# Optimization experiments

Measured on AMD Instinct MI355X. Metric: run time of the kernel, lower is better.

## Reference

```python
import jax, jax.numpy as jnp
import numpy as np


def _pairwise_sq(x, y):
    # squared euclidean distances [B,N,M] via gram trick (avoids [B,N,M,D] temp)
    x2 = jnp.sum(x * x, -1)[:, :, None]
    y2 = jnp.sum(y * y, -1)[:, None, :]
    return x2 + y2 - 2.0 * jnp.einsum('bnd,bmd->bnm', x, y)


def _dtw_dp(C):
    # Subsequence DTW accumulated-cost matrix. C: [N,M].
    # D[0,:] = C[0,:] (free start anywhere in y);
    # D[i,j] = C[i,j] + min(D[i-1,j], D[i-1,j-1], D[i,j-1]).
    # Within-row recurrence D[i,j] = min(a[j], D[i,j-1] + C[i,j]) with
    # a[j] = min(D[i-1,j], D[i-1,j-1]) + C[i,j] is a min-plus prefix scan:
    # D[i,j] = S[j] + cummin(a - S)[j], S = cumsum(C[i]).
    inf = jnp.asarray(jnp.inf, C.dtype)
    def row(Dprev, Crow):
        shifted = jnp.concatenate([jnp.full((1,), inf, C.dtype), Dprev[:-1]])
        a = jnp.minimum(Dprev, shifted) + Crow
        S = jnp.cumsum(Crow)
        D = S + jax.lax.cummin(a - S)
        return D, D
    _, Dr = jax.lax.scan(row, C[0], C[1:])
    return jnp.concatenate([C[0][None], Dr], 0)


def _backtrack(D):
    # Backtrack optimal subseq-DTW path from (N-1, argmin D[-1]) to row 0.
    # Returns, per x index i, the largest y index aligned to i on the path
    # (== last occurrence kept by dict(dtw_path) in the torch code).
    N, M = D.shape
    inf = jnp.asarray(jnp.inf, D.dtype)
    j0 = jnp.argmin(D[-1]).astype(jnp.int32)
    i0 = jnp.asarray(N - 1, jnp.int32)
    yl = jnp.zeros((N,), jnp.int32).at[i0].set(j0)
    def step(carry, _):
        i, j, yl = carry
        dd = jnp.where(j > 0, D[i - 1, j - 1], inf)
        du = D[i - 1, j]
        dl = jnp.where(j > 0, D[i, j - 1], inf)
        best = jnp.minimum(jnp.minimum(dd, du), dl)
        take_d = dd == best
        take_u = (~take_d) & (du == best)
        ni = jnp.where(take_d | take_u, i - 1, i)
        nj = jnp.where(take_d, j - 1, jnp.where(take_u, j, j - 1))
        active = i > 0
        ni = jnp.where(active, ni, i)
        nj = jnp.where(active, nj, j)
        yl = jnp.where(active, yl.at[ni].max(nj), yl)
        return (ni, nj, yl), None
    (_, _, yl), _ = jax.lax.scan(step, (i0, j0, yl), None, length=N + M)
    return yl


def setup_inputs() -> dict:
    key = jax.random.key(0)
    k0, k1, k2, k3 = jax.random.split(key, 4)
    B, N, M, D = 16, 1024, 4096, 64
    return {
        'x': jax.random.normal(k0, (B, N, D), jnp.float32),
        'y': jax.random.normal(k1, (B, M, D), jnp.float32),
        'x_t': jax.random.uniform(k2, (B, N), dtype=jnp.float32),
        'y_t': jax.random.uniform(k3, (B, M), dtype=jnp.float32),
    }


def reference(x, y, x_t, y_t):
    C = _pairwise_sq(x, y)                      # [B,N,M]
    D = jax.vmap(_dtw_dp)(C)                    # [B,N,M]
    # total path cost == DP optimum (sum of C along the optimal path)
    dtw_cost = jnp.min(D[:, -1, :], axis=-1)    # [B]
    y_last = jax.vmap(_backtrack)(jax.lax.stop_gradient(D))  # [B,N] int32
    w_ts = x_t                                  # path covers all x indices 0..N-1 in order
    w_vs = jnp.take_along_axis(y_t, y_last, axis=1)
    return dtw_cost, w_ts, w_vs
```

## Files before the change

### kernel.cpp

```cpp
#include <hip/hip_runtime.h>

#define B_ 16
#define N_ 1024
#define M_ 4096
#define D_ 64
#define SROWS_ (N_ + 63)
#define SROWSP_ (SROWS_ + 17)
#define SPAIR_ 544
#define TSB_ ((size_t)SPAIR_ * 128)
#define BTQ_ 96
#define BTROWS_ 128
#define GEMM_BLKS_ 2048

__device__ __forceinline__ float finf() { return __builtin_inff(); }

__device__ __forceinline__ float wave_shr1(float x) {
  return __int_as_float(__builtin_amdgcn_update_dpp(
      0, __float_as_int(x), 0x138, 0xF, 0xF, false));
}
__device__ __forceinline__ float rdlane(float v, int l) {
  return __int_as_float(__builtin_amdgcn_readlane(__float_as_int(v), l));
}

__global__ void prep_kernel(const float* __restrict__ x,
                            const float* __restrict__ x_t,
                            float* __restrict__ x2,
                            float* __restrict__ w_ts_out,
                            int* __restrict__ ctrl) {
  int id = blockIdx.x * blockDim.x + threadIdx.x;
  if (ctrl && blockIdx.x == 0 && threadIdx.x < 128)
    ctrl[threadIdx.x] = (threadIdx.x < 64) ? 0 : -1;
  const float4* xr = (const float4*)(x + (size_t)id * D_);
  float s = 0.f;
#pragma unroll
  for (int e = 0; e < D_ / 4; ++e) {
    float4 v = xr[e];
    s += v.x * v.x + v.y * v.y + v.z * v.z + v.w * v.w;
  }
  x2[id] = s;
  w_ts_out[id] = x_t[id];
}

__device__ __forceinline__ void gemm_body(
    const float* __restrict__ x, const float* __restrict__ y,
    const float* __restrict__ x2, float* __restrict__ CsT, int jcol0,
    int b, int ibeg, int t, char* smem) {
  float4* ylds = (float4*)smem;
  float4* xlds = (float4*)(smem + 65536);
  float* y2lds = (float*)(smem + 73728);

  const int cg = t & 63;
  const int rg = t >> 6;
  {
    const int j = jcol0 + t;
    const float4* yrow = (const float4*)(y + ((size_t)b * M_ + j) * D_);
    float4 yr[16];
#pragma unroll
    for (int e = 0; e < 16; ++e) yr[e] = yrow[e];
    float y2 = 0.f;
#pragma unroll
    for (int e = 0; e < 16; ++e)
      y2 += yr[e].x * yr[e].x + yr[e].y * yr[e].y + yr[e].z * yr[e].z +
            yr[e].w * yr[e].w;
    y2lds[t] = y2;
#pragma unroll
    for (int e = 0; e < 16; ++e) ylds[e * 256 + t] = yr[e];
  }
  if (t < 128) {
    const int row = t >> 2;
    const int part = t & 3;
    const float4* xr = (const float4*)(x + ((size_t)b * N_ + ibeg + row) * D_);
#pragma unroll
    for (int k = 0; k < 4; ++k) {
      const int e = part * 4 + k;
      xlds[e * 32 + row] = xr[e];
    }
  }
  __syncthreads();

  const int r0 = rg * 8;
  float acc[8][4];
#pragma unroll
  for (int r = 0; r < 8; ++r)
#pragma unroll
    for (int c = 0; c < 4; ++c) acc[r][c] = 0.f;

#pragma unroll
  for (int kb = 0; kb < 4; ++kb) {
    float4 yf[4][4];
#pragma unroll
    for (int c = 0; c < 4; ++c)
#pragma unroll
      for (int ee = 0; ee < 4; ++ee)
        yf[c][ee] = ylds[(kb * 4 + ee) * 256 + cg + 64 * c];
#pragma unroll
    for (int r = 0; r < 8; ++r) {
      float4 xv[4];
#pragma unroll
      for (int ee = 0; ee < 4; ++ee)
        xv[ee] = xlds[(kb * 4 + ee) * 32 + r0 + r];
#pragma unroll
      for (int ee = 0; ee < 4; ++ee) {
#pragma unroll
        for (int c = 0; c < 4; ++c) {
          acc[r][c] += xv[ee].x * yf[c][ee].x + xv[ee].y * yf[c][ee].y +
                       xv[ee].z * yf[c][ee].z + xv[ee].w * yf[c][ee].w;
        }
      }
    }
  }

#pragma unroll
  for (int r = 0; r < 8; ++r) {
    const int i = ibeg + r0 + r;
    const float xx = x2[b * N_ + i];
#pragma unroll
    for (int c = 0; c < 4; ++c) {
      const int ct = cg + 64 * c;
      const int l = ct >> 2;
      CsT[(size_t)(i + l) * 256 + ct] = xx + y2lds[ct] - 2.f * acc[r][c];
    }
  }
}

__global__ __launch_bounds__(256) void gemm_kernel(
    const float* __restrict__ x, const float* __restrict__ y,
    const float* __restrict__ x2, float* __restrict__ Cs, int chunkBase,
    int nt, int tileOff) {
  __shared__ __align__(16) char smem[74752];
  const int tile = blockIdx.x;
  const int b = blockIdx.z;
  float* CsT =
      Cs + ((size_t)b * nt + tileOff + tile) * SROWSP_ * 256;
  gemm_body(x, y, x2, CsT, chunkBase + tile * 256, b, blockIdx.y * 32,
            threadIdx.x, smem);
}

__global__ __launch_bounds__(256) void dtw_pipe(
    const float* __restrict__ x, const float* __restrict__ y,
    const float* __restrict__ x2, float* __restrict__ Cs,
    unsigned char* __restrict__ dec, float* __restrict__ carryPipe,
    int* __restrict__ gemmCnt, int* __restrict__ carryProg,
    float* __restrict__ partV, int* __restrict__ partJ) {
  __shared__ __align__(16) char smem[90112];
  const int bid = blockIdx.x;
  const int t = threadIdx.x;

  if (bid >= 64) {
    const int gb = bid - 64;
    const int chunk = 1 + (gb >> 11);
    const int g2 = gb & 2047;
    const int b = g2 >> 7;
    const int tile = g2 & 3;
    const int ibeg = ((g2 >> 2) & 31) * 32;
    float* CsT =
        Cs + ((size_t)b * 16 + chunk * 4 + tile) * SROWSP_ * 256;
    gemm_body(x, y, x2, CsT, chunk * 1024 + tile * 256, b, ibeg, t, smem);
    __syncthreads();
    if (t == 0) {
      __threadfence();
      atomicAdd(&gemmCnt[b * 4 + chunk], 1);
    }
    return;
  }

  const int b = bid >> 2;
  const int C = bid & 3;
  const int lane = t & 63;
  const int W = t >> 6;

  float(*ring)[1024] = reinterpret_cast<float(*)[1024]>(smem);
  int* prog = reinterpret_cast<int*>(smem + 12288);
  float* redV = reinterpret_cast<float*>(smem + 12352);
  int* redJ = reinterpret_cast<int*>(smem + 12384);
  volatile int* vProg = prog;

  if (t < 3) prog[t] = -1;

  if (C > 0) {
    if (t == 0) {
      while (__hip_atomic_load(&gemmCnt[b * 4 + C], __ATOMIC_ACQUIRE,
                               __HIP_MEMORY_SCOPE_AGENT) < 128)
        __builtin_amdgcn_s_sleep(8);
      __threadfence();
    }
    __syncthreads();
  } else {
    __syncthreads();
  }

  const float INF = finf();
  const float* loadP = Cs + ((size_t)b * 16 + C * 4 + W) * SROWSP_ * 256;
  const int tileG = C * 4 + W;
  unsigned short* decP =
      (unsigned short*)(dec + (size_t)(b * 16 + tileG) * TSB_) + lane;
  const float* carryIn = carryPipe + ((size_t)b * 3 + (C > 0 ? C - 1 : 0)) * N_;
  float* carryOut = carryPipe + ((size_t)b * 3 + (C < 3 ? C : 0)) * N_;
  int* progIn = &carryProg[b * 4 + (C > 0 ? C - 1 : 0)];
  int* progOut = &carryProg[b * 4 + C];
  const int jbase = tileG * 256 + lane * 4;

  float4 cc0 = ((const float4*)(loadP + 0 * 256))[lane];
  float4 cc1 = ((const float4*)(loadP + 1 * 256))[lane];
  float4 cc2 = ((const float4*)(loadP + 2 * 256))[lane];
  float4 cc3 = ((const float4*)(loadP + 3 * 256))[lane];
  float4 cc4 = ((const float4*)(loadP + 4 * 256))[lane];
  float4 cc5 = ((const float4*)(loadP + 5 * 256))[lane];
  float4 cc6 = ((const float4*)(loadP + 6 * 256))[lane];
  float4 cc7 = ((const float4*)(loadP + 7 * 256))[lane];
  loadP += 8 * 256;

  float edgeVec = INF, lvPrev = INF;
  float up0 = 0.f, up1 = 0.f, up2 = 0.f, up3 = 0.f;
  float dpp1 = INF, dpp2 = INF;
  float fin0 = INF, fin1 = INF, fin2 = INF, fin3 = INF;
  float ebuf[8];

#define BLOCKHEADP()                                                          \
  {                                                                           \
    if (W > 0) {                                                              \
      if (sb < N_) {                                                          \
        const int tgt = sb + 7;                                               \
        while (vProg[W - 1] < tgt) {}                                         \
        asm volatile("" ::: "memory");                                        \
        lvPrev = rdlane(edgeVec, 7);                                          \
        edgeVec = ring[W - 1][(sb + lane) & 1023];                            \
      }                                                                       \
    } else if (C > 0) {                                                       \
      if (((sb & 63) == 0) && sb < N_) {                                      \
        const int tgt = sb + 63;                                              \
        if (lane == 0) {                                                      \
          while (__hip_atomic_load(progIn, __ATOMIC_ACQUIRE,                  \
                                   __HIP_MEMORY_SCOPE_AGENT) < tgt)           \
            __builtin_amdgcn_s_sleep(4);                                      \
        }                                                                     \
        edgeVec = carryIn[(sb + lane) & 1023];                                \
      }                                                                       \
    }                                                                         \
  }

#define DPSTEP(KK, CCV, ROW0, FIN)                                            \
  {                                                                           \
    const float lv = rdlane(edgeVec, eb + (KK));                              \
    const float left = (lane == 0) ? lv : dpp1;                               \
    const float diag = (lane == 0) ? lvPrev : dpp2;                           \
    lvPrev = lv;                                                              \
    float bv0 = fminf(diag, fminf(up0, left));                                \
    unsigned int pk = (diag <= bv0) ? 0u : ((up0 <= bv0) ? 1u : 2u);          \
    if (ROW0) bv0 = (sb + (KK) == lane) ? 0.f : bv0;                          \
    const float D0 = CCV.x + bv0;                                             \
    float bv1 = fminf(up0, fminf(up1, D0));                                   \
    pk |= (up0 <= bv1) ? 0u : ((up1 <= bv1) ? 4u : 8u);                       \
    if (ROW0) bv1 = (sb + (KK) == lane) ? 0.f : bv1;                          \
    const float D1 = CCV.y + bv1;                                             \
    float bv2 = fminf(up1, fminf(up2, D1));                                   \
    pk |= (up1 <= bv2) ? 0u : ((up2 <= bv2) ? 16u : 32u);                     \
    if (ROW0) bv2 = (sb + (KK) == lane) ? 0.f : bv2;                          \
    const float D2 = CCV.z + bv2;                                             \
    float bv3 = fminf(up2, fminf(up3, D2));                                   \
    pk |= (up2 <= bv3) ? 0u : ((up3 <= bv3) ? 64u : 128u);                    \
    if (ROW0) bv3 = (sb + (KK) == lane) ? 0.f : bv3;                          \
    const float D3 = CCV.w + bv3;                                             \
    ebuf[(KK)] = D3;                                                          \
    if ((KK) & 1) {                                                           \
      pk16 |= pk << 8;                                                        \
      decP[((KK) >> 1) * 64] = (unsigned short)pk16;                          \
    } else {                                                                  \
      pk16 = pk;                                                              \
    }                                                                         \
    if (FIN) {                                                                \
      const bool lr = (sb + (KK) == 1023 + lane);                             \
      fin0 = lr ? D0 : fin0; fin1 = lr ? D1 : fin1;                           \
      fin2 = lr ? D2 : fin2; fin3 = lr ? D3 : fin3;                           \
    }                                                                         \
    const float sh = wave_shr1(D3);                                           \
    dpp2 = dpp1; dpp1 = sh;                                                   \
    up0 = D0; up1 = D1; up2 = D2; up3 = D3;                                   \
    CCV = ((const float4*)(loadP + (KK) * 256))[lane];                        \
  }

#define BLOCKENDP()                                                           \
  {                                                                           \
    const int r0 = sb - 63;                                                   \
    if (W < 3) {                                                              \
      if (lane == 63 && r0 > -8 && r0 < N_) {                                 \
        _Pragma("unroll") for (int k = 0; k < 8; ++k) {                       \
          const int r = r0 + k;                                               \
          if ((unsigned)r < (unsigned)N_) ring[W][r] = ebuf[k];               \
        }                                                                     \
        __builtin_amdgcn_s_waitcnt(0xC07F);                                   \
        vProg[W] = r0 + 7;                                                    \
      }                                                                       \
    } else if (C < 3) {                                                       \
      if (lane == 63) {                                                       \
        if (r0 > -8 && r0 < N_) {                                             \
          _Pragma("unroll") for (int k = 0; k < 8; ++k) {                     \
            const int r = r0 + k;                                             \
            if ((unsigned)r < (unsigned)N_) carryOut[r] = ebuf[k];            \
          }                                                                   \
        }                                                                     \
        if ((sb & 63) == 56)                                                  \
          __hip_atomic_store(progOut, sb - 56, __ATOMIC_RELEASE,              \
                             __HIP_MEMORY_SCOPE_AGENT);                       \
      }                                                                       \
    }                                                                         \
    loadP += 8 * 256;                                                         \
    decP += 256;                                                              \
  }

#define STEP8(R0, FN)                                                         \
  DPSTEP(0, cc0, R0, FN) DPSTEP(1, cc1, R0, FN) DPSTEP(2, cc2, R0, FN)        \
  DPSTEP(3, cc3, R0, FN) DPSTEP(4, cc4, R0, FN) DPSTEP(5, cc5, R0, FN)        \
  DPSTEP(6, cc6, R0, FN) DPSTEP(7, cc7, R0, FN)

  int sb = 0;
  for (; sb < 64; sb += 8) {
    BLOCKHEADP();
    const int eb = (W == 0) ? (sb & 56) : 0;
    unsigned int pk16;
    STEP8(1, 0)
    BLOCKENDP();
  }
  for (; sb < 1016; sb += 8) {
    BLOCKHEADP();
    const int eb = (W == 0) ? (sb & 56) : 0;
    unsigned int pk16;
    STEP8(0, 0)
    BLOCKENDP();
  }
  for (; sb < 1088; sb += 8) {
    BLOCKHEADP();
    const int eb = (W == 0) ? (sb & 56) : 0;
    unsigned int pk16;
    STEP8(0, 1)
    BLOCKENDP();
  }
#undef DPSTEP
#undef STEP8
#undef BLOCKHEADP
#undef BLOCKENDP

  float mv = fin0; int mj = jbase;
  if (fin1 < mv) { mv = fin1; mj = jbase + 1; }
  if (fin2 < mv) { mv = fin2; mj = jbase + 2; }
  if (fin3 < mv) { mv = fin3; mj = jbase + 3; }
#pragma unroll
  for (int off = 32; off > 0; off >>= 1) {
    const float ov = __shfl_down(mv, off);
    const int oj = __shfl_down(mj, off);
    if (ov < mv || (ov == mv && oj < mj)) { mv = ov; mj = oj; }
  }
  if (lane == 0) { redV[W] = mv; redJ[W] = mj; }
  __syncthreads();
  if (t == 0) {
    float bm = redV[0]; int bj = redJ[0];
#pragma unroll
    for (int w = 1; w < 4; ++w)
      if (redV[w] < bm) { bm = redV[w]; bj = redJ[w]; }
    partV[b * 4 + C] = bm;
    partJ[b * 4 + C] = bj;
  }
}

__global__ __launch_bounds__(256) void dtw_fused(
    const float* __restrict__ x, const float* __restrict__ y,
    const float* __restrict__ x2, const float* __restrict__ CsRead,
    float* __restrict__ CsWrite, int nextBase,
    unsigned char* __restrict__ dec, const float* __restrict__ carryIn,
    float* __restrict__ carryOut, float* __restrict__ partV,
    int* __restrict__ partJ, int chunk, int hasCarry) {
  __shared__ __align__(16) char smem[90112];
  const int bid = blockIdx.x;
  const int t = threadIdx.x;

  if (bid >= B_) {
    const int gb = bid - B_;
    const int b = gb >> 7;
    const int tile = gb & 3;
    const int ibeg = ((gb >> 2) & 31) * 32;
    float* CsT = CsWrite + ((size_t)b * 4 + tile) * SROWSP_ * 256;
    gemm_body(x, y, x2, CsT, nextBase + tile * 256, b, ibeg, t, smem);
    return;
  }

  float(*ring)[1024] = reinterpret_cast<float(*)[1024]>(smem);
  float* cring = reinterpret_cast<float*>(smem + 12288);
  int* prog = reinterpret_cast<int*>(smem + 16384);
  float* redV = reinterpret_cast<float*>(smem + 16400);
  int* redJ = reinterpret_cast<int*>(smem + 16416);
  volatile int* vProg = prog;

  const int b = bid;
  const int lane = t & 63;
  const int W = t >> 6;

  if (t < 3) prog[t] = -1;
  const float* cIn = carryIn + b * N_;
  if (hasCarry) ((float4*)cring)[t] = ((const float4*)cIn)[t];
  __syncthreads();

  const float INF = finf();
  const float* loadP = CsRead + (size_t)(b * 4 + W) * SROWSP_ * 256;
  const int tileG = chunk * 4 + W;
  unsigned short* decP =
      (unsigned short*)(dec + (size_t)(b * 16 + tileG) * TSB_) + lane;
  float* carryB = carryOut + b * N_;
  const int jbase = tileG * 256 + lane * 4;

  float4 cc0 = ((const float4*)(loadP + 0 * 256))[lane];
  float4 cc1 = ((const float4*)(loadP + 1 * 256))[lane];
  float4 cc2 = ((const float4*)(loadP + 2 * 256))[lane];
  float4 cc3 = ((const float4*)(loadP + 3 * 256))[lane];
  float4 cc4 = ((const float4*)(loadP + 4 * 256))[lane];
  float4 cc5 = ((const float4*)(loadP + 5 * 256))[lane];
  float4 cc6 = ((const float4*)(loadP + 6 * 256))[lane];
  float4 cc7 = ((const float4*)(loadP + 7 * 256))[lane];
  loadP += 8 * 256;

  float edgeVec = INF, lvPrev = INF;
  float up0 = 0.f, up1 = 0.f, up2 = 0.f, up3 = 0.f;
  float dpp1 = INF, dpp2 = INF;
  float fin0 = INF, fin1 = INF, fin2 = INF, fin3 = INF;
  float ebuf[8];

#define BLOCKHEAD()                                                           \
  {                                                                           \
    if (W > 0) {                                                              \
      if (sb < N_) {                                                          \
        const int tgt = sb + 7;                                               \
        while (vProg[W - 1] < tgt) {}                                         \
        asm volatile("" ::: "memory");                                        \
        lvPrev = rdlane(edgeVec, 7);                                          \
        edgeVec = ring[W - 1][(sb + lane) & 1023];                            \
      }                                                                       \
    } else if (hasCarry) {                                                    \
      lvPrev = rdlane(edgeVec, 7);                                            \
      if (sb < N_) edgeVec = cring[(sb + lane) & 1023];                       \
    }                                                                         \
  }

#define DPSTEP(KK, CCV, ROW0, FIN)                                            \
  {                                                                           \
    const float lv = rdlane(edgeVec, (KK));                                   \
    const float left = (lane == 0) ? lv : dpp1;                               \
    const float diag = (lane == 0) ? lvPrev : dpp2;                           \
    lvPrev = lv;                                                              \
    float bv0 = fminf(diag, fminf(up0, left));                                \
    unsigned int pk = (diag <= bv0) ? 0u : ((up0 <= bv0) ? 1u : 2u);          \
    if (ROW0) bv0 = (sb + (KK) == lane) ? 0.f : bv0;                          \
    const float D0 = CCV.x + bv0;                                             \
    float bv1 = fminf(up0, fminf(up1, D0));                                   \
    pk |= (up0 <= bv1) ? 0u : ((up1 <= bv1) ? 4u : 8u);                       \
    if (ROW0) bv1 = (sb + (KK) == lane) ? 0.f : bv1;                          \
    const float D1 = CCV.y + bv1;                                             \
    float bv2 = fminf(up1, fminf(up2, D1));                                   \
    pk |= (up1 <= bv2) ? 0u : ((up2 <= bv2) ? 16u : 32u);                     \
    if (ROW0) bv2 = (sb + (KK) == lane) ? 0.f : bv2;                          \
    const float D2 = CCV.z + bv2;                                             \
    float bv3 = fminf(up2, fminf(up3, D2));                                   \
    pk |= (up2 <= bv3) ? 0u : ((up3 <= bv3) ? 64u : 128u);                    \
    if (ROW0) bv3 = (sb + (KK) == lane) ? 0.f : bv3;                          \
    const float D3 = CCV.w + bv3;                                             \
    ebuf[(KK)] = D3;                                                          \
    if ((KK) & 1) {                                                           \
      pk16 |= pk << 8;                                                        \
      decP[((KK) >> 1) * 64] = (unsigned short)pk16;                          \
    } else {                                                                  \
      pk16 = pk;                                                              \
    }                                                                         \
    if (FIN) {                                                                \
      const bool lr = (sb + (KK) == 1023 + lane);                             \
      fin0 = lr ? D0 : fin0; fin1 = lr ? D1 : fin1;                           \
      fin2 = lr ? D2 : fin2; fin3 = lr ? D3 : fin3;                           \
    }                                                                         \
    const float sh = wave_shr1(D3);                                           \
    dpp2 = dpp1; dpp1 = sh;                                                   \
    up0 = D0; up1 = D1; up2 = D2; up3 = D3;                                   \
    CCV = ((const float4*)(loadP + (KK) * 256))[lane];                        \
  }

#define BLOCKEND()                                                            \
  {                                                                           \
    const int r0 = sb - 63;                                                   \
    if (W < 3) {                                                              \
      if (lane == 63 && r0 > -8 && r0 < N_) {                                 \
        _Pragma("unroll") for (int k = 0; k < 8; ++k) {                       \
          const int r = r0 + k;                                               \
          if ((unsigned)r < (unsigned)N_) ring[W][r] = ebuf[k];               \
        }                                                                     \
        __builtin_amdgcn_s_waitcnt(0xC07F);                                   \
        vProg[W] = r0 + 7;                                                    \
      }                                                                       \
    } else if (chunk < 3) {                                                   \
      if (lane == 63 && r0 > -8 && r0 < N_) {                                 \
        _Pragma("unroll") for (int k = 0; k < 8; ++k) {                       \
          const int r = r0 + k;                                               \
          if ((unsigned)r < (unsigned)N_) carryB[r] = ebuf[k];                \
        }                                                                     \
      }                                                                       \
    }                                                                         \
    loadP += 8 * 256;                                                         \
    decP += 256;                                                              \
  }

#define STEP8(R0, FN)                                                         \
  DPSTEP(0, cc0, R0, FN) DPSTEP(1, cc1, R0, FN) DPSTEP(2, cc2, R0, FN)        \
  DPSTEP(3, cc3, R0, FN) DPSTEP(4, cc4, R0, FN) DPSTEP(5, cc5, R0, FN)        \
  DPSTEP(6, cc6, R0, FN) DPSTEP(7, cc7, R0, FN)

  int sb = 0;
  for (; sb < 64; sb += 8) {
    BLOCKHEAD();
    unsigned int pk16;
    STEP8(1, 0)
    BLOCKEND();
  }
  for (; sb < 1016; sb += 8) {
    BLOCKHEAD();
    unsigned int pk16;
    STEP8(0, 0)
    BLOCKEND();
  }
  for (; sb < 1088; sb += 8) {
    BLOCKHEAD();
    unsigned int pk16;
    STEP8(0, 1)
    BLOCKEND();
  }
#undef DPSTEP
#undef STEP8
#undef BLOCKHEAD
#undef BLOCKEND

  float mv = fin0; int mj = jbase;
  if (fin1 < mv) { mv = fin1; mj = jbase + 1; }
  if (fin2 < mv) { mv = fin2; mj = jbase + 2; }
  if (fin3 < mv) { mv = fin3; mj = jbase + 3; }
#pragma unroll
  for (int off = 32; off > 0; off >>= 1) {
    const float ov = __shfl_down(mv, off);
    const int oj = __shfl_down(mj, off);
    if (ov < mv || (ov == mv && oj < mj)) { mv = ov; mj = oj; }
  }
  if (lane == 0) { redV[W] = mv; redJ[W] = mj; }
  __syncthreads();
  if (t == 0) {
    float bm = redV[0]; int bj = redJ[0];
#pragma unroll
    for (int w = 1; w < 4; ++w)
      if (redV[w] < bm) { bm = redV[w]; bj = redJ[w]; }
    partV[b * 4 + chunk] = bm;
    partJ[b * 4 + chunk] = bj;
  }
}

__global__ __launch_bounds__(64) void backtrack_kernel(
    const unsigned char* __restrict__ dec, const float* __restrict__ partV,
    const int* __restrict__ partJ, int nch, const float* __restrict__ y_t,
    float* __restrict__ w_vs, float* __restrict__ cost_out) {
  const int b = blockIdx.x;
  const int lane = threadIdx.x;
  __shared__ unsigned int stage[3 * 3072];
  __shared__ unsigned short tab[BTROWS_][BTQ_ * 4 + 2];
  __shared__ int st_i, st_j;
  __shared__ int jrow[BTROWS_ + 1];
  const unsigned char* db = dec + (size_t)b * 16 * TSB_;
  const float* yt = y_t + b * M_;
  float* wv = w_vs + b * N_;

  if (lane == 0) {
    float bc = finf(); int bj = 0;
    for (int c = 0; c < nch; ++c) {
      const float v = partV[b * nch + c];
      const int j = partJ[b * nch + c];
      if (v < bc) { bc = v; bj = j; }
    }
    cost_out[b] = bc;
    st_i = N_ - 1;
    st_j = bj;
    wv[N_ - 1] = yt[bj];
  }
  for (;;) {
    __syncthreads();
    const int i = st_i, j = st_j;
    if (i <= 0) break;
    const int qj = j >> 2;
    int qlo = qj - (BTQ_ - 1);
    if (qlo < 0) qlo = 0;
    const int Tbase = qlo >> 6;
    int plo = (i - 127) >> 1;
    if (plo < 0) plo = 0;

#pragma unroll
    for (int tt = 0; tt < 3; ++tt) {
      int T = Tbase + tt;
      if (T > 15) T = 15;
      const uint4* src =
          (const uint4*)(db + (size_t)T * TSB_ + (size_t)plo * 128);
#pragma unroll
      for (int v = 0; v < 12; ++v) {
        const int wb = tt * 12288 + (v * 64 + lane) * 16;
        const int sw = wb ^ (((wb >> 7) & 7) << 4);
        *(uint4*)((char*)stage + sw) = src[v * 64 + lane];
      }
    }
    __syncthreads();

    const unsigned char* sb8 = (const unsigned char*)stage;
#pragma unroll
    for (int half = 0; half < 2; ++half) {
      const int r = i - lane - half * 64;
      if (r >= 1) {
        unsigned char wr[BTQ_];
#pragma unroll
        for (int k = 0; k < BTQ_; ++k) {
          const int q = qlo + k;
          const int tt = (q >> 6) - Tbase;
          const int l = q & 63;
          const int s = r + l;
          int idx = tt * 12288 + ((s >> 1) - plo) * 128 + l * 2 + (s & 1);
          idx ^= ((idx >> 7) & 7) << 4;
          wr[k] = sb8[idx];
        }
        unsigned short run = 0xFFFF;
        const int tr = lane + half * 64;
#pragma unroll
        for (int k = 0; k < BTQ_; ++k) {
          const unsigned int byte = wr[k];
#pragma unroll
          for (int cs = 0; cs < 4; ++cs) {
            const unsigned int code = (byte >> (2 * cs)) & 3u;
            const int c = 4 * k + cs;
            const unsigned short v =
                (code != 2u) ? (unsigned short)((c << 2) | code) : run;
            tab[tr][c] = v;
            run = v;
          }
        }
      }
    }
    __syncthreads();
    if (lane == 0) {
      const int base = qlo << 2;
      int rr = i, cj = j;
      while (rr >= 1 && (i - rr) < BTROWS_) {
        const int l = i - rr;
        const int c = cj - base;
        if (c < 0) break;
        const unsigned short v = tab[l][c];
        if (v == 0xFFFF) { cj = base - 1; break; }
        const int e = v >> 2;
        const int ce = v & 3;
        cj = base + e - (ce == 0 ? 1 : 0);
        --rr;
        jrow[i - rr] = cj;
      }
      st_i = rr;
      st_j = cj;
    }
    __syncthreads();
    const int cnt = i - st_i;
    if (lane < cnt) wv[i - 1 - lane] = yt[jrow[lane + 1]];
    {
      const int l2 = lane + 64;
      if (l2 < cnt) wv[i - 1 - l2] = yt[jrow[l2 + 1]];
    }
  }
}

extern "C" void kernel_launch(void* const* d_in, const int* in_sizes, int n_in,
                              void* d_out, int out_size, void* d_ws, size_t ws_size,
                              hipStream_t stream) {
  const float* x = (const float*)d_in[0];
  const float* y = (const float*)d_in[1];
  const float* x_t = (const float*)d_in[2];
  const float* y_t = (const float*)d_in[3];

  float* out_cost = (float*)d_out;
  float* out_wts = out_cost + B_;
  float* out_wvs = out_wts + B_ * N_;

  const size_t csChunk = (size_t)B_ * 4 * SROWSP_ * 256 * 4;
  const size_t csFull = (size_t)B_ * 16 * SROWSP_ * 256 * 4;
  const size_t decBytes = (size_t)B_ * 16 * TSB_;
  const size_t x2Bytes = (size_t)B_ * N_ * 4;
  const size_t pipeTail = x2Bytes + 3 * (size_t)B_ * N_ * 4 + 4096;
  const size_t r6Tail = x2Bytes + 2 * (size_t)B_ * N_ * 4 + B_ * 4 * 8;

  char* ws = (char*)d_ws;

  if (ws_size >= csFull + decBytes + pipeTail) {
    float* Cs = (float*)ws;
    unsigned char* dec = (unsigned char*)(ws + csFull);
    float* x2 = (float*)(ws + csFull + decBytes);
    float* carryPipe = x2 + B_ * N_;
    float* partV = carryPipe + 3 * B_ * N_;
    int* partJ = (int*)(partV + 64);
    int* ctrl = partJ + 64;

    prep_kernel<<<dim3((B_ * N_) / 256), 256, 0, stream>>>(x, x_t, x2,
                                                           out_wts, ctrl);
    gemm_kernel<<<dim3(4, N_ / 32, B_), 256, 0, stream>>>(x, y, x2, Cs, 0,
                                                          16, 0);
    dtw_pipe<<<dim3(64 + 3 * GEMM_BLKS_), 256, 0, stream>>>(
        x, y, x2, Cs, dec, carryPipe, ctrl, ctrl + 64, partV, partJ);
    backtrack_kernel<<<dim3(B_), 64, 0, stream>>>(dec, partV, partJ, 4, y_t,
                                                  out_wvs, out_cost);
    return;
  }

  const int overlap = ws_size >= 2 * csChunk + decBytes + r6Tail;
  const int nCs = overlap ? 2 : 1;
  float* CsA = (float*)ws;
  float* CsB = overlap ? (float*)(ws + csChunk) : CsA;
  unsigned char* dec = (unsigned char*)(ws + (size_t)nCs * csChunk);
  float* x2 = (float*)(ws + (size_t)nCs * csChunk + decBytes);
  float* carryA = x2 + B_ * N_;
  float* carryB = carryA + B_ * N_;
  float* partV = carryB + B_ * N_;
  int* partJ = (int*)(partV + B_ * 4);

  prep_kernel<<<dim3((B_ * N_) / 256), 256, 0, stream>>>(x, x_t, x2, out_wts,
                                                         nullptr);

  float* cbuf[2] = {carryA, carryB};
  if (overlap) {
    gemm_kernel<<<dim3(4, N_ / 32, B_), 256, 0, stream>>>(x, y, x2, CsA, 0,
                                                          4, 0);
    for (int c = 0; c < 4; ++c) {
      float* csR = (c & 1) ? CsB : CsA;
      float* csW = (c & 1) ? CsA : CsB;
      const int nblk = B_ + (c < 3 ? GEMM_BLKS_ : 0);
      dtw_fused<<<dim3(nblk), 256, 0, stream>>>(
          x, y, x2, csR, csW, (c + 1) * 1024, dec, cbuf[(c + 1) & 1],
          cbuf[c & 1], partV, partJ, c, c > 0 ? 1 : 0);
    }
  } else {
    for (int c = 0; c < 4; ++c) {
      gemm_kernel<<<dim3(4, N_ / 32, B_), 256, 0, stream>>>(x, y, x2, CsA,
                                                            c * 1024, 4, 0);
      dtw_fused<<<dim3(B_), 256, 0, stream>>>(
          x, y, x2, CsA, CsA, 0, dec, cbuf[(c + 1) & 1], cbuf[c & 1], partV,
          partJ, c, c > 0 ? 1 : 0);
    }
  }

  backtrack_kernel<<<dim3(B_), 64, 0, stream>>>(dec, partV, partJ, 4, y_t,
                                                out_wvs, out_cost);
}
```

Measured before the change: 1.009 ms.

## Replace separate GEMM launch with persistent work-queue workers and ring buffer

The chunk-0 GEMM kernel launch is removed. All cost-matrix tiles are now produced by a fixed pool of persistent worker blocks, which pull jobs from an atomic queue inside the DTW pipeline kernel. Cost buffers become a ring of 2 to 4 chunk slots sized to the available workspace. Workers wait for the DTW consumer to release a slot (tracked with per-chunk done flags), and DTW blocks now wait on the GEMM count for chunk 0 as well. The goal is to overlap the first GEMM with DTW startup, reduce workspace footprint and launch overhead, and shrink the row-padding stride. The cost is spin-wait dependencies that could stall progress or deadlock if residency assumptions fail.

```diff
diff --git a/kernel.cpp b/kernel.cpp
--- a/kernel.cpp
+++ b/kernel.cpp
@@ -5,11 +5,14 @@
 #define M_ 4096
 #define D_ 64
 #define SROWS_ (N_ + 63)
-#define SROWSP_ (SROWS_ + 17)
+#define SROWSP_ (SROWS_ + 9)
 #define SPAIR_ 544
 #define TSB_ ((size_t)SPAIR_ * 128)
 #define BTQ_ 96
 #define BTROWS_ 128
+#define CSF_ ((size_t)B_ * 4 * SROWSP_ * 256)
+#define NJOBS_ 8192
+#define NWORK_ 176
 #define GEMM_BLKS_ 2048
 
 __device__ __forceinline__ float finf() { return __builtin_inff(); }
@@ -28,8 +31,10 @@
                             float* __restrict__ w_ts_out,
                             int* __restrict__ ctrl) {
   int id = blockIdx.x * blockDim.x + threadIdx.x;
-  if (ctrl && blockIdx.x == 0 && threadIdx.x < 128)
-    ctrl[threadIdx.x] = (threadIdx.x < 64) ? 0 : -1;
+  if (ctrl && blockIdx.x == 0) {
+    const int v = (threadIdx.x >= 128 && threadIdx.x < 192) ? -1 : 0;
+    ctrl[threadIdx.x] = v;
+  }
   const float4* xr = (const float4*)(x + (size_t)id * D_);
   float s = 0.f;
 #pragma unroll
@@ -125,41 +130,56 @@
 
 __global__ __launch_bounds__(256) void gemm_kernel(
     const float* __restrict__ x, const float* __restrict__ y,
-    const float* __restrict__ x2, float* __restrict__ Cs, int chunkBase,
-    int nt, int tileOff) {
+    const float* __restrict__ x2, float* __restrict__ Cs, int chunkBase) {
   __shared__ __align__(16) char smem[74752];
   const int tile = blockIdx.x;
   const int b = blockIdx.z;
-  float* CsT =
-      Cs + ((size_t)b * nt + tileOff + tile) * SROWSP_ * 256;
+  float* CsT = Cs + ((size_t)b * 4 + tile) * SROWSP_ * 256;
   gemm_body(x, y, x2, CsT, chunkBase + tile * 256, b, blockIdx.y * 32,
             threadIdx.x, smem);
 }
 
 __global__ __launch_bounds__(256) void dtw_pipe(
     const float* __restrict__ x, const float* __restrict__ y,
-    const float* __restrict__ x2, float* __restrict__ Cs,
+    const float* __restrict__ x2, float* __restrict__ Cs, int nbuf,
     unsigned char* __restrict__ dec, float* __restrict__ carryPipe,
-    int* __restrict__ gemmCnt, int* __restrict__ carryProg,
-    float* __restrict__ partV, int* __restrict__ partJ) {
+    int* __restrict__ ctrl, float* __restrict__ partV,
+    int* __restrict__ partJ) {
   __shared__ __align__(16) char smem[90112];
   const int bid = blockIdx.x;
   const int t = threadIdx.x;
+  int* GD = ctrl;
+  int* DPD = ctrl + 64;
+  int* CPRG = ctrl + 128;
+  int* QH = ctrl + 192;
 
   if (bid >= 64) {
-    const int gb = bid - 64;
-    const int chunk = 1 + (gb >> 11);
-    const int g2 = gb & 2047;
-    const int b = g2 >> 7;
-    const int tile = g2 & 3;
-    const int ibeg = ((g2 >> 2) & 31) * 32;
-    float* CsT =
-        Cs + ((size_t)b * 16 + chunk * 4 + tile) * SROWSP_ * 256;
-    gemm_body(x, y, x2, CsT, chunk * 1024 + tile * 256, b, ibeg, t, smem);
-    __syncthreads();
-    if (t == 0) {
-      __threadfence();
-      atomicAdd(&gemmCnt[b * 4 + chunk], 1);
+    volatile int* jslot = (int*)(smem + 81920);
+    for (;;) {
+      __syncthreads();
+      if (t == 0) *jslot = atomicAdd(QH, 1);
+      __syncthreads();
+      const int j = *jslot;
+      if (j >= NJOBS_) break;
+      const int c = j >> 11;
+      const int r2 = j & 2047;
+      const int b = r2 >> 7;
+      const int tile = (r2 >> 5) & 3;
+      const int rb = r2 & 31;
+      if (t == 0 && c >= nbuf) {
+        while (!__hip_atomic_load(&DPD[b * 4 + c - nbuf], __ATOMIC_ACQUIRE,
+                                  __HIP_MEMORY_SCOPE_AGENT))
+          __builtin_amdgcn_s_sleep(8);
+      }
+      __syncthreads();
+      float* CsT = Cs + (size_t)(c % nbuf) * CSF_ +
+                   ((size_t)b * 4 + tile) * SROWSP_ * 256;
+      gemm_body(x, y, x2, CsT, c * 1024 + tile * 256, b, rb * 32, t, smem);
+      __syncthreads();
+      if (t == 0) {
+        __threadfence();
+        atomicAdd(&GD[b * 4 + c], 1);
+      }
     }
     return;
   }
@@ -176,28 +196,24 @@
   volatile int* vProg = prog;
 
   if (t < 3) prog[t] = -1;
-
-  if (C > 0) {
-    if (t == 0) {
-      while (__hip_atomic_load(&gemmCnt[b * 4 + C], __ATOMIC_ACQUIRE,
-                               __HIP_MEMORY_SCOPE_AGENT) < 128)
-        __builtin_amdgcn_s_sleep(8);
-      __threadfence();
-    }
-    __syncthreads();
-  } else {
-    __syncthreads();
-  }
+  if (t == 0) {
+    while (__hip_atomic_load(&GD[b * 4 + C], __ATOMIC_ACQUIRE,
+                             __HIP_MEMORY_SCOPE_AGENT) < 128)
+      __builtin_amdgcn_s_sleep(8);
+    __threadfence();
+  }
+  __syncthreads();
 
   const float INF = finf();
-  const float* loadP = Cs + ((size_t)b * 16 + C * 4 + W) * SROWSP_ * 256;
+  const float* loadP = Cs + (size_t)(C % nbuf) * CSF_ +
+                       ((size_t)b * 4 + W) * SROWSP_ * 256;
   const int tileG = C * 4 + W;
   unsigned short* decP =
       (unsigned short*)(dec + (size_t)(b * 16 + tileG) * TSB_) + lane;
   const float* carryIn = carryPipe + ((size_t)b * 3 + (C > 0 ? C - 1 : 0)) * N_;
   float* carryOut = carryPipe + ((size_t)b * 3 + (C < 3 ? C : 0)) * N_;
-  int* progIn = &carryProg[b * 4 + (C > 0 ? C - 1 : 0)];
-  int* progOut = &carryProg[b * 4 + C];
+  int* progIn = &CPRG[b * 4 + (C > 0 ? C - 1 : 0)];
+  int* progOut = &CPRG[b * 4 + C];
   const int jbase = tileG * 256 + lane * 4;
 
   float4 cc0 = ((const float4*)(loadP + 0 * 256))[lane];
@@ -359,6 +375,8 @@
       if (redV[w] < bm) { bm = redV[w]; bj = redJ[w]; }
     partV[b * 4 + C] = bm;
     partJ[b * 4 + C] = bj;
+    __hip_atomic_store(&DPD[b * 4 + C], 1, __ATOMIC_RELEASE,
+                       __HIP_MEMORY_SCOPE_AGENT);
   }
 }
 
@@ -680,19 +698,22 @@
   float* out_wts = out_cost + B_;
   float* out_wvs = out_wts + B_ * N_;
 
-  const size_t csChunk = (size_t)B_ * 4 * SROWSP_ * 256 * 4;
-  const size_t csFull = (size_t)B_ * 16 * SROWSP_ * 256 * 4;
+  const size_t csChunk = CSF_ * sizeof(float);
   const size_t decBytes = (size_t)B_ * 16 * TSB_;
   const size_t x2Bytes = (size_t)B_ * N_ * 4;
-  const size_t pipeTail = x2Bytes + 3 * (size_t)B_ * N_ * 4 + 4096;
-  const size_t r6Tail = x2Bytes + 2 * (size_t)B_ * N_ * 4 + B_ * 4 * 8;
+  const size_t pipeTail = x2Bytes + 3 * (size_t)B_ * N_ * 4 + 8192;
 
   char* ws = (char*)d_ws;
 
-  if (ws_size >= csFull + decBytes + pipeTail) {
+  int nbuf = 0;
+  for (int k = 4; k >= 2; --k) {
+    if (ws_size >= (size_t)k * csChunk + decBytes + pipeTail) { nbuf = k; break; }
+  }
+
+  if (nbuf >= 2) {
     float* Cs = (float*)ws;
-    unsigned char* dec = (unsigned char*)(ws + csFull);
-    float* x2 = (float*)(ws + csFull + decBytes);
+    unsigned char* dec = (unsigned char*)(ws + (size_t)nbuf * csChunk);
+    float* x2 = (float*)(ws + (size_t)nbuf * csChunk + decBytes);
     float* carryPipe = x2 + B_ * N_;
     float* partV = carryPipe + 3 * B_ * N_;
     int* partJ = (int*)(partV + 64);
@@ -700,15 +721,14 @@
 
     prep_kernel<<<dim3((B_ * N_) / 256), 256, 0, stream>>>(x, x_t, x2,
                                                            out_wts, ctrl);
-    gemm_kernel<<<dim3(4, N_ / 32, B_), 256, 0, stream>>>(x, y, x2, Cs, 0,
-                                                          16, 0);
-    dtw_pipe<<<dim3(64 + 3 * GEMM_BLKS_), 256, 0, stream>>>(
-        x, y, x2, Cs, dec, carryPipe, ctrl, ctrl + 64, partV, partJ);
+    dtw_pipe<<<dim3(64 + NWORK_), 256, 0, stream>>>(
+        x, y, x2, Cs, nbuf, dec, carryPipe, ctrl, partV, partJ);
     backtrack_kernel<<<dim3(B_), 64, 0, stream>>>(dec, partV, partJ, 4, y_t,
                                                   out_wvs, out_cost);
     return;
   }
 
+  const size_t r6Tail = x2Bytes + 2 * (size_t)B_ * N_ * 4 + B_ * 4 * 8;
   const int overlap = ws_size >= 2 * csChunk + decBytes + r6Tail;
   const int nCs = overlap ? 2 : 1;
   float* CsA = (float*)ws;
@@ -725,8 +745,7 @@
 
   float* cbuf[2] = {carryA, carryB};
   if (overlap) {
-    gemm_kernel<<<dim3(4, N_ / 32, B_), 256, 0, stream>>>(x, y, x2, CsA, 0,
-                                                          4, 0);
+    gemm_kernel<<<dim3(4, N_ / 32, B_), 256, 0, stream>>>(x, y, x2, CsA, 0);
     for (int c = 0; c < 4; ++c) {
       float* csR = (c & 1) ? CsB : CsA;
       float* csW = (c & 1) ? CsA : CsB;
@@ -738,7 +757,7 @@
   } else {
     for (int c = 0; c < 4; ++c) {
       gemm_kernel<<<dim3(4, N_ / 32, B_), 256, 0, stream>>>(x, y, x2, CsA,
-                                                            c * 1024, 4, 0);
+                                                            c * 1024);
       dtw_fused<<<dim3(B_), 256, 0, stream>>>(
           x, y, x2, CsA, CsA, 0, dec, cbuf[(c + 1) & 1], cbuf[c & 1], partV,
           partJ, c, c > 0 ? 1 : 0);
```

Result: slower. 1.350 ms (+33.8%).
